# Kernel tuning notes

Measured on AMD Instinct MI355X. Metric: run time of the kernel, lower is better.

## Reference

```python
import jax, jax.numpy as jnp
import numpy as np

QDEPTH = 10
W, H = 32, 32
PIXELS = W * H          # 1024
WIRES = 10              # ceil(log2(1024))
BATCH = 1024


def _rot(phi, theta, omega):
    """PennyLane Rot = RZ(omega) RY(theta) RZ(phi), as a 2x2 complex matrix."""
    c = jnp.cos(theta * 0.5).astype(jnp.complex64)
    s = jnp.sin(theta * 0.5).astype(jnp.complex64)
    ep = jnp.exp(-0.5j * (phi + omega))  # e^{-i(phi+omega)/2}
    em = jnp.exp(-0.5j * (phi - omega))  # e^{-i(phi-omega)/2}
    return jnp.stack([
        jnp.stack([ep * c, -jnp.conj(em) * s]),
        jnp.stack([em * s, jnp.conj(ep) * c]),
    ])


def _apply_1q(state, gate, wire):
    # state: [B, 2, 2, ..., 2] (WIRES qubit axes, wire 0 is most significant)
    s = jnp.tensordot(gate, state, axes=((1,), (wire + 1,)))
    return jnp.moveaxis(s, 0, wire + 1)


def _apply_cnot(state, ctrl, tgt):
    ac, at = ctrl + 1, tgt + 1
    s0 = jax.lax.index_in_dim(state, 0, axis=ac, keepdims=True)
    s1 = jax.lax.index_in_dim(state, 1, axis=ac, keepdims=True)
    return jnp.concatenate([s0, jnp.flip(s1, axis=at)], axis=ac)


def _forward(x, weights):
    b = x.shape[0]
    feats = x.reshape(b, PIXELS)
    # AmplitudeEmbedding with normalize=True (pixels == 2**WIRES, no padding needed)
    norm = jnp.sqrt(jnp.sum(feats * feats, axis=1, keepdims=True))
    state = (feats / norm).astype(jnp.complex64)
    state = state.reshape((b,) + (2,) * WIRES)

    tw = jnp.tanh(weights)  # [QDEPTH, WIRES, 3]
    for l in range(QDEPTH):
        for q in range(WIRES):
            g = _rot(tw[l, q, 0], tw[l, q, 1], tw[l, q, 2])
            state = _apply_1q(state, g, q)
        r = (l % (WIRES - 1)) + 1  # StronglyEntanglingLayers default ranges
        for q in range(WIRES):
            state = _apply_cnot(state, q, (q + r) % WIRES)

    probs = jnp.abs(state.reshape(b, -1)) ** 2  # qml.probs
    probs = jnp.clip(probs[:, :PIXELS] * PIXELS, 0.0, 1.0)
    return probs.reshape(b, 1, W, H)


def setup_inputs() -> dict:
    key = jax.random.key(0)
    k1, k2 = jax.random.split(key)
    x = jax.random.uniform(k1, (BATCH, 1, W, H), dtype=jnp.float32)
    weights = jax.random.normal(k2, (QDEPTH, WIRES, 3), dtype=jnp.float32) * 0.4
    return {"x": x, "weights": weights}


def reference(x, weights):
    return _forward(x, weights)
```

## Files before the change

### kernel.cpp

```cpp
#include <hip/hip_runtime.h>
#include <math.h>
#include <type_traits>

#define QDEPTH 10
#define WIRES 10
#define NSTATE 1024
#define NGATES (QDEPTH * WIRES)

typedef float f2 __attribute__((ext_vector_type(2)));
typedef float f4 __attribute__((ext_vector_type(4)));

constexpr unsigned sigma_apply(int q, int r, unsigned i) {
    int cb = 9 - q, tb = 9 - ((q + r) % 10);
    return i ^ (((i >> cb) & 1u) << tb);
}
constexpr unsigned G_apply(int l, unsigned i) {
    int r = (l % 9) + 1;
    for (int q = 9; q >= 0; --q) i = sigma_apply(q, r, i);
    return i;
}

struct FoldT { unsigned short e[QDEPTH][64][16]; };
constexpr FoldT make_fold() {
    FoldT t{};
    for (int l = 0; l < QDEPTH; ++l)
        for (unsigned lane = 0; lane < 64; ++lane)
            for (unsigned j = 0; j < 16; ++j) {
                unsigned s = (j << 6) | lane;
                unsigned h = G_apply(l, s);
                unsigned d = h & ~4u;
                unsigned a_half = ((d >> 3) << 2) | (d & 3u);
                t.e[l][lane][j] = (unsigned short)(a_half | (((h >> 2) & 1u) << 15));
            }
    return t;
}
__constant__ FoldT FOLD = make_fold();

template <int N, int I = 0, typename F>
__device__ __forceinline__ void static_for(F&& f) {
    if constexpr (I < N) {
        f(std::integral_constant<int, I>{});
        static_for<N, I + 1>(f);
    }
}

__device__ __forceinline__ float fxor(float a, unsigned s) {
    return __uint_as_float(__float_as_uint(a) ^ s);
}
__device__ __forceinline__ f2 fxor2(f2 a, unsigned s) {
    f2 r; r.x = fxor(a.x, s); r.y = fxor(a.y, s); return r;
}
__device__ __forceinline__ f2 swap2(f2 a) { return __builtin_shufflevector(a, a, 1, 0); }
__device__ __forceinline__ f2 pkfma(f2 a, f2 b, f2 c) {
    return __builtin_elementwise_fma(a, b, c);
}

__global__ void gates_kernel(const float* __restrict__ w, float* __restrict__ g) {
    int i = threadIdx.x;
    if (i >= NGATES) return;
    float phi = tanhf(w[3 * i + 0]);
    float th  = tanhf(w[3 * i + 1]);
    float om  = tanhf(w[3 * i + 2]);
    float c = cosf(0.5f * th), s = sinf(0.5f * th);
    float a = 0.5f * (phi + om), d = 0.5f * (phi - om);
    float Ar =  cosf(a) * c, Ai = -sinf(a) * c;
    float Br = -cosf(d) * s, Bi = -sinf(d) * s;
    float* p = g + 8 * i;
    p[0] = Ar;  p[1] = Ar;
    p[2] = -Ai; p[3] = Ai;
    p[4] = Br;  p[5] = Br;
    p[6] = -Bi; p[7] = Bi;
}

template <int JB>
__device__ __forceinline__ void apply_gate_reg(f2 (&s)[16], f2 ArP, f2 AiSW,
                                               f2 BrP, f2 BiSW) {
    static_for<8>([&](auto P) {
        constexpr int p  = P.value;
        constexpr int lo = p & ((1 << JB) - 1);
        constexpr int j  = ((p & ~((1 << JB) - 1)) << 1) | lo;
        constexpr int jp = j | (1 << JB);
        f2 a = s[j], b = s[jp];
        f2 as = swap2(a), bs = swap2(b);
        f2 n0 = a * ArP;
        n0 = pkfma(AiSW, as, n0); n0 = pkfma(BrP, b, n0); n0 = pkfma(BiSW, bs, n0);
        f2 n1 = a * (-BrP);
        n1 = pkfma(BiSW, as, n1); n1 = pkfma(ArP, b, n1); n1 = pkfma(-AiSW, bs, n1);
        s[j] = n0; s[jp] = n1;
    });
}

template <bool IS32>
__device__ __forceinline__ void plane_gate(f2& v, f2& w, f2 ArP, f2 AiSW,
                                           f2 BrP, f2 BiSW) {
    unsigned vx = __float_as_uint(v.x), vy = __float_as_uint(v.y);
    unsigned wx = __float_as_uint(w.x), wy = __float_as_uint(w.y);
    unsigned Xx, Xy, Yx, Yy;
    if constexpr (IS32) {
        auto rx = __builtin_amdgcn_permlane32_swap(vx, wx, false, false);
        auto ry = __builtin_amdgcn_permlane32_swap(vy, wy, false, false);
        Xx = rx[0]; Yx = rx[1]; Xy = ry[0]; Yy = ry[1];
    } else {
        auto rx = __builtin_amdgcn_permlane16_swap(vx, wx, false, false);
        auto ry = __builtin_amdgcn_permlane16_swap(vy, wy, false, false);
        Xx = rx[0]; Yx = rx[1]; Xy = ry[0]; Yy = ry[1];
    }
    f2 X, Y;
    X.x = __uint_as_float(Xx); X.y = __uint_as_float(Xy);
    Y.x = __uint_as_float(Yx); Y.y = __uint_as_float(Yy);
    f2 as = swap2(X), bs = swap2(Y);
    f2 n0 = X * ArP;
    n0 = pkfma(AiSW, as, n0); n0 = pkfma(BrP, Y, n0); n0 = pkfma(BiSW, bs, n0);
    f2 n1 = X * (-BrP);
    n1 = pkfma(BiSW, as, n1); n1 = pkfma(ArP, Y, n1); n1 = pkfma(-AiSW, bs, n1);
    unsigned ax = __float_as_uint(n0.x), ay = __float_as_uint(n0.y);
    unsigned bx = __float_as_uint(n1.x), by = __float_as_uint(n1.y);
    if constexpr (IS32) {
        auto ox = __builtin_amdgcn_permlane32_swap(ax, bx, false, false);
        auto oy = __builtin_amdgcn_permlane32_swap(ay, by, false, false);
        v.x = __uint_as_float(ox[0]); v.y = __uint_as_float(oy[0]);
        w.x = __uint_as_float(ox[1]); w.y = __uint_as_float(oy[1]);
    } else {
        auto ox = __builtin_amdgcn_permlane16_swap(ax, bx, false, false);
        auto oy = __builtin_amdgcn_permlane16_swap(ay, by, false, false);
        v.x = __uint_as_float(ox[0]); v.y = __uint_as_float(oy[0]);
        w.x = __uint_as_float(ox[1]); w.y = __uint_as_float(oy[1]);
    }
}

template <int CTRL>
__device__ __forceinline__ f2 dpp2(f2 v) {
    f2 r;
    r.x = __uint_as_float((unsigned)__builtin_amdgcn_mov_dpp(
              (int)__float_as_uint(v.x), CTRL, 0xf, 0xf, true));
    r.y = __uint_as_float((unsigned)__builtin_amdgcn_mov_dpp(
              (int)__float_as_uint(v.y), CTRL, 0xf, 0xf, true));
    return r;
}

template <int CTRL, int M>
__device__ __forceinline__ void dpp_gate(f2 (&s)[16], int lane, f2 ArP, f2 AiSW,
                                         f2 BrP, f2 BiSW) {
    const unsigned sm = (lane & M) ? 0x80000000u : 0u;
    const f2 c2 = fxor2(AiSW, sm);
    const f2 c3 = fxor2(BrP, sm);
    static_for<16>([&](auto J) {
        constexpr int j = J.value;
        f2 a = s[j];
        f2 p = dpp2<CTRL>(a);
        f2 n = a * ArP;
        n = pkfma(c2, swap2(a), n);
        n = pkfma(c3, p, n);
        n = pkfma(BiSW, swap2(p), n);
        s[j] = n;
    });
}

__global__ __launch_bounds__(256) void sim_kernel(const float* __restrict__ x,
                                                  const float* __restrict__ gtab,
                                                  float* __restrict__ out) {
    __shared__ f2 amps[4][NSTATE];
    const int tid  = threadIdx.x;
    const int w    = tid >> 6;
    const int lane = tid & 63;
    const int elem = blockIdx.x * 4 + w;
    const float* xb = x + (size_t)elem * NSTATE;
    f2* myb = amps[w];
    const f2* gt = (const f2*)gtab;

    f2 s[16];

    float ss = 0.f;
    static_for<16>([&](auto J) {
        constexpr int j = J.value;
        float v = xb[(j << 6) | lane];
        s[j].x = v; s[j].y = 0.f;
        ss = fmaf(v, v, ss);
    });
#pragma unroll
    for (int off = 1; off < 64; off <<= 1) ss += __shfl_xor(ss, off);
    const float nrm = 1.0f / sqrtf(ss);
    static_for<16>([&](auto J) { s[J.value] *= nrm; });

    const int wb = ((lane >> 3) << 3) | ((lane & 3) << 1) | ((lane >> 2) & 1);

#pragma unroll 1
    for (int l = 0; l < QDEPTH; ++l) {
        const f2* gl = gt + 40 * l;

        const uint4* tp = (const uint4*)&FOLD.e[l][lane][0];
        uint4 e0 = tp[0], e1 = tp[1];
        unsigned ew[8] = { e0.x, e0.y, e0.z, e0.w, e1.x, e1.y, e1.z, e1.w };

        apply_gate_reg<3>(s, gl[0],  gl[1],  gl[2],  gl[3]);
        apply_gate_reg<2>(s, gl[4],  gl[5],  gl[6],  gl[7]);
        apply_gate_reg<1>(s, gl[8],  gl[9],  gl[10], gl[11]);
        apply_gate_reg<0>(s, gl[12], gl[13], gl[14], gl[15]);

        {
            f2 a0 = gl[16], a1 = gl[17], a2 = gl[18], a3 = gl[19];
            static_for<8>([&](auto K) {
                constexpr int k = K.value;
                plane_gate<true>(s[2 * k], s[2 * k + 1], a0, a1, a2, a3);
            });
        }
        {
            f2 a0 = gl[20], a1 = gl[21], a2 = gl[22], a3 = gl[23];
            static_for<8>([&](auto K) {
                constexpr int k = K.value;
                plane_gate<false>(s[2 * k], s[2 * k + 1], a0, a1, a2, a3);
            });
        }

        dpp_gate<0x128, 8>(s, lane, gl[24], gl[25], gl[26], gl[27]);
        dpp_gate<0x04E, 2>(s, lane, gl[32], gl[33], gl[34], gl[35]);
        dpp_gate<0x0B1, 1>(s, lane, gl[36], gl[37], gl[38], gl[39]);

        static_for<16>([&](auto J) {
            constexpr int j = J.value;
            myb[(j << 6) | wb] = s[j];
        });

        {
            const f2 ArP = gl[28], AiSW = gl[29], BrP = gl[30], BiSW = gl[31];
            static_for<16>([&](auto J) {
                constexpr int j = J.value;
                unsigned E  = (j & 1) ? (ew[j >> 1] >> 16) : (ew[j >> 1] & 0xFFFFu);
                unsigned sm = (E & 0x8000u) << 16;
                const f4 pv = *(const f4*)&myb[(E & 0x1FFu) << 1];
                f2 v0; v0.x = pv.x; v0.y = pv.y;
                f2 v1; v1.x = pv.z; v1.y = pv.w;
                bool h2 = (E & 0x8000u) != 0;
                f2 a  = h2 ? v1 : v0;
                f2 pp = h2 ? v0 : v1;
                f2 c2 = fxor2(AiSW, sm);
                f2 c3 = fxor2(BrP, sm);
                f2 n = a * ArP;
                n = pkfma(c2, swap2(a), n);
                n = pkfma(c3, pp, n);
                n = pkfma(BiSW, swap2(pp), n);
                s[j] = n;
            });
        }
    }

    float* ob = out + (size_t)elem * NSTATE;
    static_for<16>([&](auto J) {
        constexpr int j = J.value;
        float p = fmaf(s[j].x, s[j].x, s[j].y * s[j].y) * (float)NSTATE;
        ob[(j << 6) | lane] = fminf(p, 1.0f);
    });
}

extern "C" void kernel_launch(void* const* d_in, const int* in_sizes, int n_in,
                              void* d_out, int out_size, void* d_ws, size_t ws_size,
                              hipStream_t stream) {
    const float* x = (const float*)d_in[0];
    const float* w = (const float*)d_in[1];
    float* out   = (float*)d_out;
    float* gates = (float*)d_ws;

    gates_kernel<<<1, 128, 0, stream>>>(w, gates);
    sim_kernel<<<256, 256, 0, stream>>>(x, gates, out);
}
```

Measured before the change: 40.03 us.

## Split each state vector across two wavefronts with double-buffered LDS exchange

Each batch element is now simulated by two wavefronts, each holding 8 amplitudes per lane instead of 16, and the grid doubles to 512 blocks. The wire-0 gate, which now spans both waves, is folded into the LDS exchange step together with the existing LDS-routed gate. That step reads four amplitudes per output and uses double-buffered shared memory plus a block barrier each layer. Gate coefficients are staged in LDS and the norm is reduced across the two waves via shared memory. The aim is more parallelism and lower register pressure, at the cost of per-layer __syncthreads, extra LDS reads and some duplicated arithmetic.

New measurement: 44.35 us. +10.8%, slower.

```diff
diff --git a/kernel.cpp b/kernel.cpp
--- a/kernel.cpp
+++ b/kernel.cpp
@@ -8,7 +8,6 @@
 #define NGATES (QDEPTH * WIRES)
 
 typedef float f2 __attribute__((ext_vector_type(2)));
-typedef float f4 __attribute__((ext_vector_type(4)));
 
 constexpr unsigned sigma_apply(int q, int r, unsigned i) {
     int cb = 9 - q, tb = 9 - ((q + r) % 10);
@@ -19,18 +18,18 @@
     for (int q = 9; q >= 0; --q) i = sigma_apply(q, r, i);
     return i;
 }
-
-struct FoldT { unsigned short e[QDEPTH][64][16]; };
+constexpr unsigned Afun(unsigned p) {
+    return ((p >> 3) << 3) | ((p & 3u) << 1) | ((p >> 2) & 1u);
+}
+
+struct FoldT { unsigned short e[QDEPTH][128][8]; };
 constexpr FoldT make_fold() {
     FoldT t{};
     for (int l = 0; l < QDEPTH; ++l)
-        for (unsigned lane = 0; lane < 64; ++lane)
-            for (unsigned j = 0; j < 16; ++j) {
-                unsigned s = (j << 6) | lane;
-                unsigned h = G_apply(l, s);
-                unsigned d = h & ~4u;
-                unsigned a_half = ((d >> 3) << 2) | (d & 3u);
-                t.e[l][lane][j] = (unsigned short)(a_half | (((h >> 2) & 1u) << 15));
+        for (unsigned wl = 0; wl < 128; ++wl)
+            for (unsigned j = 0; j < 8; ++j) {
+                unsigned s = ((wl >> 6) << 9) | (j << 6) | (wl & 63u);
+                t.e[l][wl][j] = (unsigned short)Afun(G_apply(l, s));
             }
     return t;
 }
@@ -73,9 +72,9 @@
 }
 
 template <int JB>
-__device__ __forceinline__ void apply_gate_reg(f2 (&s)[16], f2 ArP, f2 AiSW,
+__device__ __forceinline__ void apply_gate_reg(f2 (&s)[8], f2 ArP, f2 AiSW,
                                                f2 BrP, f2 BiSW) {
-    static_for<8>([&](auto P) {
+    static_for<4>([&](auto P) {
         constexpr int p  = P.value;
         constexpr int lo = p & ((1 << JB) - 1);
         constexpr int j  = ((p & ~((1 << JB) - 1)) << 1) | lo;
@@ -139,12 +138,12 @@
 }
 
 template <int CTRL, int M>
-__device__ __forceinline__ void dpp_gate(f2 (&s)[16], int lane, f2 ArP, f2 AiSW,
+__device__ __forceinline__ void dpp_gate(f2 (&s)[8], int lane, f2 ArP, f2 AiSW,
                                          f2 BrP, f2 BiSW) {
     const unsigned sm = (lane & M) ? 0x80000000u : 0u;
     const f2 c2 = fxor2(AiSW, sm);
     const f2 c3 = fxor2(BrP, sm);
-    static_for<16>([&](auto J) {
+    static_for<8>([&](auto J) {
         constexpr int j = J.value;
         f2 a = s[j];
         f2 p = dpp2<CTRL>(a);
@@ -159,54 +158,58 @@
 __global__ __launch_bounds__(256) void sim_kernel(const float* __restrict__ x,
                                                   const float* __restrict__ gtab,
                                                   float* __restrict__ out) {
-    __shared__ f2 amps[4][NSTATE];
+    __shared__ f2 buf[2][2][NSTATE];
+    __shared__ f2 glds[NGATES * 4];
+    __shared__ float wsum[2][2];
     const int tid  = threadIdx.x;
-    const int w    = tid >> 6;
+    const int e    = tid >> 7;
+    const int w    = (tid >> 6) & 1;
     const int lane = tid & 63;
-    const int elem = blockIdx.x * 4 + w;
+    const int elem = blockIdx.x * 2 + e;
     const float* xb = x + (size_t)elem * NSTATE;
-    f2* myb = amps[w];
-    const f2* gt = (const f2*)gtab;
-
-    f2 s[16];
+
+    for (int i = tid; i < NGATES * 4; i += 256)
+        glds[i] = ((const f2*)gtab)[i];
+
+    f2 s[8];
 
     float ss = 0.f;
-    static_for<16>([&](auto J) {
+    static_for<8>([&](auto J) {
         constexpr int j = J.value;
-        float v = xb[(j << 6) | lane];
+        float v = xb[(w << 9) | (j << 6) | lane];
         s[j].x = v; s[j].y = 0.f;
         ss = fmaf(v, v, ss);
     });
 #pragma unroll
     for (int off = 1; off < 64; off <<= 1) ss += __shfl_xor(ss, off);
-    const float nrm = 1.0f / sqrtf(ss);
-    static_for<16>([&](auto J) { s[J.value] *= nrm; });
+    if (lane == 0) wsum[e][w] = ss;
+    __syncthreads();
+    const float nrm = 1.0f / sqrtf(wsum[e][0] + wsum[e][1]);
+    static_for<8>([&](auto J) { s[J.value] *= nrm; });
 
     const int wb = ((lane >> 3) << 3) | ((lane & 3) << 1) | ((lane >> 2) & 1);
 
 #pragma unroll 1
     for (int l = 0; l < QDEPTH; ++l) {
-        const f2* gl = gt + 40 * l;
-
-        const uint4* tp = (const uint4*)&FOLD.e[l][lane][0];
-        uint4 e0 = tp[0], e1 = tp[1];
-        unsigned ew[8] = { e0.x, e0.y, e0.z, e0.w, e1.x, e1.y, e1.z, e1.w };
-
-        apply_gate_reg<3>(s, gl[0],  gl[1],  gl[2],  gl[3]);
+        const f2* gl = glds + 40 * l;
+
+        const uint4 fe = *(const uint4*)&FOLD.e[l][tid & 127][0];
+        unsigned ew[4] = { fe.x, fe.y, fe.z, fe.w };
+
         apply_gate_reg<2>(s, gl[4],  gl[5],  gl[6],  gl[7]);
         apply_gate_reg<1>(s, gl[8],  gl[9],  gl[10], gl[11]);
         apply_gate_reg<0>(s, gl[12], gl[13], gl[14], gl[15]);
 
         {
             f2 a0 = gl[16], a1 = gl[17], a2 = gl[18], a3 = gl[19];
-            static_for<8>([&](auto K) {
+            static_for<4>([&](auto K) {
                 constexpr int k = K.value;
                 plane_gate<true>(s[2 * k], s[2 * k + 1], a0, a1, a2, a3);
             });
         }
         {
             f2 a0 = gl[20], a1 = gl[21], a2 = gl[22], a3 = gl[23];
-            static_for<8>([&](auto K) {
+            static_for<4>([&](auto K) {
                 constexpr int k = K.value;
                 plane_gate<false>(s[2 * k], s[2 * k + 1], a0, a1, a2, a3);
             });
@@ -216,39 +219,45 @@
         dpp_gate<0x04E, 2>(s, lane, gl[32], gl[33], gl[34], gl[35]);
         dpp_gate<0x0B1, 1>(s, lane, gl[36], gl[37], gl[38], gl[39]);
 
-        static_for<16>([&](auto J) {
+        f2* B = &buf[l & 1][e][0];
+        static_for<8>([&](auto J) {
             constexpr int j = J.value;
-            myb[(j << 6) | wb] = s[j];
+            B[(w << 9) | (j << 6) | wb] = s[j];
         });
-
-        {
-            const f2 ArP = gl[28], AiSW = gl[29], BrP = gl[30], BiSW = gl[31];
-            static_for<16>([&](auto J) {
-                constexpr int j = J.value;
-                unsigned E  = (j & 1) ? (ew[j >> 1] >> 16) : (ew[j >> 1] & 0xFFFFu);
-                unsigned sm = (E & 0x8000u) << 16;
-                const f4 pv = *(const f4*)&myb[(E & 0x1FFu) << 1];
-                f2 v0; v0.x = pv.x; v0.y = pv.y;
-                f2 v1; v1.x = pv.z; v1.y = pv.w;
-                bool h2 = (E & 0x8000u) != 0;
-                f2 a  = h2 ? v1 : v0;
-                f2 pp = h2 ? v0 : v1;
-                f2 c2 = fxor2(AiSW, sm);
-                f2 c3 = fxor2(BrP, sm);
-                f2 n = a * ArP;
-                n = pkfma(c2, swap2(a), n);
-                n = pkfma(c3, pp, n);
-                n = pkfma(BiSW, swap2(pp), n);
-                s[j] = n;
-            });
-        }
+        __syncthreads();
+
+        const f2 CrP = gl[28], CiSW = gl[29], DrP = gl[30], DiSW = gl[31];
+        const f2 ErP = gl[0],  EiSW = gl[1],  FrP = gl[2],  FiSW = gl[3];
+        static_for<8>([&](auto J) {
+            constexpr int j = J.value;
+            unsigned ks  = (j & 1) ? (ew[j >> 1] >> 16) : (ew[j >> 1] & 0xFFFFu);
+            unsigned sm2 = (ks & 1u) << 31;
+            unsigned sm9 = ((ks >> 9) & 1u) << 31;
+            f2 vS = B[ks],        vP = B[ks ^ 1u];
+            f2 wS = B[ks ^ 512u], wP = B[ks ^ 513u];
+            f2 c2 = fxor2(CiSW, sm2), c3 = fxor2(DrP, sm2);
+            f2 t1 = vS * CrP;
+            t1 = pkfma(c2, swap2(vS), t1);
+            t1 = pkfma(c3, vP, t1);
+            t1 = pkfma(DiSW, swap2(vP), t1);
+            f2 t2 = wS * CrP;
+            t2 = pkfma(c2, swap2(wS), t2);
+            t2 = pkfma(c3, wP, t2);
+            t2 = pkfma(DiSW, swap2(wP), t2);
+            f2 e2 = fxor2(EiSW, sm9), e3 = fxor2(FrP, sm9);
+            f2 n = t1 * ErP;
+            n = pkfma(e2, swap2(t1), n);
+            n = pkfma(e3, t2, n);
+            n = pkfma(FiSW, swap2(t2), n);
+            s[j] = n;
+        });
     }
 
     float* ob = out + (size_t)elem * NSTATE;
-    static_for<16>([&](auto J) {
+    static_for<8>([&](auto J) {
         constexpr int j = J.value;
         float p = fmaf(s[j].x, s[j].x, s[j].y * s[j].y) * (float)NSTATE;
-        ob[(j << 6) | lane] = fminf(p, 1.0f);
+        ob[(w << 9) | (j << 6) | lane] = fminf(p, 1.0f);
     });
 }
 
@@ -261,5 +270,5 @@
     float* gates = (float*)d_ws;
 
     gates_kernel<<<1, 128, 0, stream>>>(w, gates);
-    sim_kernel<<<256, 256, 0, stream>>>(x, gates, out);
-}
+    sim_kernel<<<512, 256, 0, stream>>>(x, gates, out);
+}
```
